# Kernel tuning notes

Hardware: AMD Instinct MI355X
Metric: run time of the kernel (lower is better)

Reference implementation:

```python
import jax, jax.numpy as jnp
import numpy as np

BATCH, S, N_DIM, B_SIZE = 512, 66, 304, 128

def setup_inputs() -> dict:
    key = jax.random.key(0)
    kx, kw = jax.random.split(key)
    x = jax.random.normal(kx, (BATCH, S, N_DIM), dtype=jnp.float32)
    W = jax.random.normal(kw, (B_SIZE, N_DIM), dtype=jnp.float32) * (1.0 / np.sqrt(N_DIM))
    b = jnp.zeros((B_SIZE,), dtype=jnp.float32)
    return {"x": x, "W": W, "b": b}

def reference(x, W, b):
    # Linear projection into tree space: (batch, S, B_size)
    t = jnp.einsum('bsd,kd->bsk', x, W) + b
    # Pairwise squared distances over sentence positions, same math as
    # expand/transpose/subtract/pow(2)/sum in the torch module.
    diff = t[:, :, None, :] - t[:, None, :, :]        # (batch, S, S, B_size)
    return jnp.sum(diff * diff, axis=-1)               # (batch, S, S)
```

## Files before the change

### kernel.cpp

```cpp
#include <hip/hip_runtime.h>
#include <hip/hip_bf16.h>

#define NBATCH 512
#define NS 66
#define ND 304
#define NK 128

#define XROWS 80
#define XSTRIDE_B 640
#define XBYTES (XROWS * XSTRIDE_B)
#define TSTRIDE_B 256
#define TBYTES (XROWS * TSTRIDE_B)
#define GSTRIDE 84

#define NTHREADS 512

typedef __attribute__((ext_vector_type(8))) short bf16x8;
typedef __attribute__((ext_vector_type(4))) short s16x4;
typedef __attribute__((ext_vector_type(4))) float f32x4;

__device__ __forceinline__ short f2bf(float x) {
    return __builtin_bit_cast(short, __float2bfloat16(x));
}

__global__ __launch_bounds__(NTHREADS, 4) void treeprobe_mfma(
    const float* __restrict__ x,
    const float* __restrict__ W,
    float* __restrict__ out)
{
    __shared__ __align__(16) char lds[XBYTES + TBYTES];
    char* const t_lds = lds + XBYTES;
    float* const G = (float*)lds;

    const int tid   = threadIdx.x;
    const int batch = blockIdx.x;
    const int lane  = tid & 63;
    const int wv    = tid >> 6;
    const int lr    = lane & 15;
    const int lg    = lane >> 4;

    bf16x8 wfrag[10];
    {
        const int c = wv * 16 + lr;
        const float* __restrict__ wr = W + c * ND;
#pragma unroll
        for (int kk = 0; kk < 10; ++kk) {
            const int k0 = kk * 32 + lg * 8;
            bf16x8 f = {0, 0, 0, 0, 0, 0, 0, 0};
            if (k0 < ND) {
                const float4 p0 = *reinterpret_cast<const float4*>(wr + k0);
                const float4 p1 = *reinterpret_cast<const float4*>(wr + k0 + 4);
                f[0] = f2bf(p0.x); f[1] = f2bf(p0.y);
                f[2] = f2bf(p0.z); f[3] = f2bf(p0.w);
                f[4] = f2bf(p1.x); f[5] = f2bf(p1.y);
                f[6] = f2bf(p1.z); f[7] = f2bf(p1.w);
            }
            wfrag[kk] = f;
        }
    }

    for (int i = tid; i < XBYTES / 16; i += NTHREADS) {
        *reinterpret_cast<f32x4*>(lds + i * 16) = (f32x4){0.f, 0.f, 0.f, 0.f};
    }
    __syncthreads();

    const float* __restrict__ xb = x + (size_t)batch * NS * ND;
    for (int e = tid; e < NS * ND / 4; e += NTHREADS) {
        const int s  = e / 76;
        const int d4 = (e % 76) * 4;
        const float4 v = *reinterpret_cast<const float4*>(xb + e * 4);
        int byte = s * XSTRIDE_B + d4 * 2;
        byte ^= (s & 7) << 4;
        s16x4 sv;
        sv[0] = f2bf(v.x); sv[1] = f2bf(v.y);
        sv[2] = f2bf(v.z); sv[3] = f2bf(v.w);
        *reinterpret_cast<s16x4*>(lds + byte) = sv;
    }
    __syncthreads();

    f32x4 acc[5];
#pragma unroll
    for (int mt = 0; mt < 5; ++mt) acc[mt] = (f32x4){0.f, 0.f, 0.f, 0.f};

#pragma unroll
    for (int kk = 0; kk < 10; ++kk) {
        bf16x8 a[5];
#pragma unroll
        for (int mt = 0; mt < 5; ++mt) {
            const int row = mt * 16 + lr;
            int byte = row * XSTRIDE_B + kk * 64 + lg * 16;
            byte ^= (row & 7) << 4;
            a[mt] = *reinterpret_cast<const bf16x8*>(lds + byte);
        }
#pragma unroll
        for (int mt = 0; mt < 5; ++mt)
            acc[mt] = __builtin_amdgcn_mfma_f32_16x16x32_bf16(
                a[mt], wfrag[kk], acc[mt], 0, 0, 0);
    }

    {
        const int col = wv * 16 + lr;
#pragma unroll
        for (int mt = 0; mt < 5; ++mt) {
#pragma unroll
            for (int r = 0; r < 4; ++r) {
                const int row = mt * 16 + lg * 4 + r;
                int byte = row * TSTRIDE_B + col * 2;
                byte ^= (row & 7) << 4;
                *reinterpret_cast<short*>(t_lds + byte) = f2bf(acc[mt][r]);
            }
        }
    }
    __syncthreads();

    for (int tile = wv; tile < 25; tile += 8) {
        const int ti = tile / 5, tj = tile % 5;
        f32x4 g = (f32x4){0.f, 0.f, 0.f, 0.f};
#pragma unroll
        for (int kk = 0; kk < 4; ++kk) {
            const int ra = ti * 16 + lr;
            int ba = ra * TSTRIDE_B + kk * 64 + lg * 16;
            ba ^= (ra & 7) << 4;
            const int rb = tj * 16 + lr;
            int bb = rb * TSTRIDE_B + kk * 64 + lg * 16;
            bb ^= (rb & 7) << 4;
            const bf16x8 av = *reinterpret_cast<const bf16x8*>(t_lds + ba);
            const bf16x8 bv = *reinterpret_cast<const bf16x8*>(t_lds + bb);
            g = __builtin_amdgcn_mfma_f32_16x16x32_bf16(av, bv, g, 0, 0, 0);
        }
#pragma unroll
        for (int r = 0; r < 4; ++r) {
            const int row = ti * 16 + lg * 4 + r;
            const int col = tj * 16 + lr;
            G[row * GSTRIDE + col] = g[r];
        }
    }
    __syncthreads();

    float* __restrict__ ob = out + (size_t)batch * NS * NS;
    for (int e = tid; e < NS * NS / 2; e += NTHREADS) {
        const int i = e / 33;
        const int j = (e % 33) * 2;
        const float nii = G[i * GSTRIDE + i];
        float2 r;
        r.x = nii + G[j * GSTRIDE + j] - 2.f * G[i * GSTRIDE + j];
        r.y = nii + G[(j + 1) * GSTRIDE + (j + 1)] - 2.f * G[i * GSTRIDE + j + 1];
        *reinterpret_cast<float2*>(ob + i * NS + j) = r;
    }
}

extern "C" void kernel_launch(void* const* d_in, const int* in_sizes, int n_in,
                              void* d_out, int out_size, void* d_ws, size_t ws_size,
                              hipStream_t stream) {
    const float* x = (const float*)d_in[0];
    const float* W = (const float*)d_in[1];
    float* out = (float*)d_out;

    treeprobe_mfma<<<NBATCH, NTHREADS, 0, stream>>>(x, W, out);
}
```

Before: 21.26 us.

## Pipeline x/W loads over K-chunks and exploit Gram symmetry with register epilogue

The kernel now uses 256 threads and splits the projection into ten K-chunks of 32. Global loads for x and W are issued two chunks ahead into registers and staged through a double-buffered LDS slice, so memory traffic overlaps the MFMA work and the LDS footprint shrinks. The Gram stage computes only the 15 upper-triangular 16x16 tiles and records the diagonal norms in a small array. Output is written straight from registers, with mirrored stores for off-diagonal tiles, replacing the full G matrix in LDS. The cost is more complex control flow, uncoalesced transposed stores, and reloading W from global per chunk instead of keeping it in registers.

```diff
diff --git a/kernel.cpp b/kernel.cpp
--- a/kernel.cpp
+++ b/kernel.cpp
@@ -5,15 +5,14 @@
 #define NS 66
 #define ND 304
 #define NK 128
-
-#define XROWS 80
-#define XSTRIDE_B 640
-#define XBYTES (XROWS * XSTRIDE_B)
+#define NTHREADS 256
+#define NCHUNK 10
+
+#define CSTRIDE_B 64
+#define CBYTES (80 * CSTRIDE_B)
 #define TSTRIDE_B 256
-#define TBYTES (XROWS * TSTRIDE_B)
-#define GSTRIDE 84
-
-#define NTHREADS 512
+#define TBYTES (80 * TSTRIDE_B)
+#define NE 528
 
 typedef __attribute__((ext_vector_type(8))) short bf16x8;
 typedef __attribute__((ext_vector_type(4))) short s16x4;
@@ -23,14 +22,19 @@
     return __builtin_bit_cast(short, __float2bfloat16(x));
 }
 
-__global__ __launch_bounds__(NTHREADS, 4) void treeprobe_mfma(
+__device__ const int TI_LUT[15] = {0,1,2,3,4, 0,0,0,0,1,1,1,2,2,3};
+__device__ const int TJ_LUT[15] = {0,1,2,3,4, 1,2,3,4,2,3,4,3,4,4};
+
+#define LDS_BARRIER() asm volatile("s_waitcnt lgkmcnt(0)\n\ts_barrier" ::: "memory")
+
+__global__ __launch_bounds__(NTHREADS, 2) void treeprobe_mfma(
     const float* __restrict__ x,
     const float* __restrict__ W,
     float* __restrict__ out)
 {
-    __shared__ __align__(16) char lds[XBYTES + TBYTES];
-    char* const t_lds = lds + XBYTES;
-    float* const G = (float*)lds;
+    __shared__ __align__(16) char xlds[2 * CBYTES];
+    __shared__ __align__(16) char t_lds[TBYTES];
+    __shared__ float norms[80];
 
     const int tid   = threadIdx.x;
     const int batch = blockIdx.x;
@@ -39,114 +43,183 @@
     const int lr    = lane & 15;
     const int lg    = lane >> 4;
 
-    bf16x8 wfrag[10];
-    {
-        const int c = wv * 16 + lr;
-        const float* __restrict__ wr = W + c * ND;
-#pragma unroll
-        for (int kk = 0; kk < 10; ++kk) {
-            const int k0 = kk * 32 + lg * 8;
-            bf16x8 f = {0, 0, 0, 0, 0, 0, 0, 0};
-            if (k0 < ND) {
-                const float4 p0 = *reinterpret_cast<const float4*>(wr + k0);
-                const float4 p1 = *reinterpret_cast<const float4*>(wr + k0 + 4);
-                f[0] = f2bf(p0.x); f[1] = f2bf(p0.y);
-                f[2] = f2bf(p0.z); f[3] = f2bf(p0.w);
-                f[4] = f2bf(p1.x); f[5] = f2bf(p1.y);
-                f[6] = f2bf(p1.z); f[7] = f2bf(p1.w);
-            }
-            wfrag[kk] = f;
-        }
-    }
-
-    for (int i = tid; i < XBYTES / 16; i += NTHREADS) {
-        *reinterpret_cast<f32x4*>(lds + i * 16) = (f32x4){0.f, 0.f, 0.f, 0.f};
-    }
-    __syncthreads();
-
     const float* __restrict__ xb = x + (size_t)batch * NS * ND;
-    for (int e = tid; e < NS * ND / 4; e += NTHREADS) {
-        const int s  = e / 76;
-        const int d4 = (e % 76) * 4;
-        const float4 v = *reinterpret_cast<const float4*>(xb + e * 4);
-        int byte = s * XSTRIDE_B + d4 * 2;
-        byte ^= (s & 7) << 4;
-        s16x4 sv;
-        sv[0] = f2bf(v.x); sv[1] = f2bf(v.y);
-        sv[2] = f2bf(v.z); sv[3] = f2bf(v.w);
-        *reinterpret_cast<s16x4*>(lds + byte) = sv;
-    }
-    __syncthreads();
-
-    f32x4 acc[5];
-#pragma unroll
-    for (int mt = 0; mt < 5; ++mt) acc[mt] = (f32x4){0.f, 0.f, 0.f, 0.f};
-
-#pragma unroll
-    for (int kk = 0; kk < 10; ++kk) {
-        bf16x8 a[5];
-#pragma unroll
-        for (int mt = 0; mt < 5; ++mt) {
-            const int row = mt * 16 + lr;
-            int byte = row * XSTRIDE_B + kk * 64 + lg * 16;
-            byte ^= (row & 7) << 4;
-            a[mt] = *reinterpret_cast<const bf16x8*>(lds + byte);
-        }
-#pragma unroll
-        for (int mt = 0; mt < 5; ++mt)
-            acc[mt] = __builtin_amdgcn_mfma_f32_16x16x32_bf16(
-                a[mt], wfrag[kk], acc[mt], 0, 0, 0);
-    }
-
-    {
-        const int col = wv * 16 + lr;
-#pragma unroll
-        for (int mt = 0; mt < 5; ++mt) {
+
+#define ISSUE_X(xr, c)                                                        \
+    _Pragma("unroll")                                                         \
+    for (int i = 0; i < 3; ++i) {                                             \
+        const int e = tid + i * NTHREADS;                                     \
+        float4 v = make_float4(0.f, 0.f, 0.f, 0.f);                           \
+        if (e < NE) {                                                         \
+            const int kc = (c) * 32 + (e & 7) * 4;                            \
+            if (kc < ND)                                                      \
+                v = *reinterpret_cast<const float4*>(xb + (e >> 3) * ND + kc);\
+        }                                                                     \
+        xr[i] = v;                                                            \
+    }
+
+#define ISSUE_W(wr4, c)                                                       \
+    _Pragma("unroll")                                                         \
+    for (int nt = 0; nt < 2; ++nt) {                                          \
+        const int row = (wv * 2 + nt) * 16 + lr;                              \
+        const int k0 = (c) * 32 + lg * 8;                                     \
+        if (k0 < ND) {                                                        \
+            wr4[nt * 2]     = *reinterpret_cast<const float4*>(W + row * ND + k0);     \
+            wr4[nt * 2 + 1] = *reinterpret_cast<const float4*>(W + row * ND + k0 + 4); \
+        } else {                                                              \
+            wr4[nt * 2]     = make_float4(0.f, 0.f, 0.f, 0.f);                \
+            wr4[nt * 2 + 1] = make_float4(0.f, 0.f, 0.f, 0.f);                \
+        }                                                                     \
+    }
+
+#define WRITE_X(xr, buf)                                                      \
+    _Pragma("unroll")                                                         \
+    for (int i = 0; i < 3; ++i) {                                             \
+        const int e = tid + i * NTHREADS;                                     \
+        if (e < NE) {                                                         \
+            const int row = e >> 3;                                           \
+            const int byte = row * CSTRIDE_B                                  \
+                + (((((e & 7) >> 1) ^ (row & 3)) << 4) | ((e & 1) << 3));     \
+            s16x4 sv;                                                         \
+            sv[0] = f2bf(xr[i].x); sv[1] = f2bf(xr[i].y);                     \
+            sv[2] = f2bf(xr[i].z); sv[3] = f2bf(xr[i].w);                     \
+            *reinterpret_cast<s16x4*>(xlds + (buf) * CBYTES + byte) = sv;     \
+        }                                                                     \
+    }
+
+#define CVT_W(wfrag, wr4)                                                     \
+    _Pragma("unroll")                                                         \
+    for (int nt = 0; nt < 2; ++nt) {                                          \
+        bf16x8 f;                                                             \
+        f[0] = f2bf(wr4[nt * 2].x);     f[1] = f2bf(wr4[nt * 2].y);           \
+        f[2] = f2bf(wr4[nt * 2].z);     f[3] = f2bf(wr4[nt * 2].w);           \
+        f[4] = f2bf(wr4[nt * 2 + 1].x); f[5] = f2bf(wr4[nt * 2 + 1].y);       \
+        f[6] = f2bf(wr4[nt * 2 + 1].z); f[7] = f2bf(wr4[nt * 2 + 1].w);       \
+        wfrag[nt] = f;                                                        \
+    }
+
+    float4 xr0[3], xr1[3], wr0[4], wr1[4];
+    ISSUE_X(xr0, 0); ISSUE_W(wr0, 0);
+    ISSUE_X(xr1, 1); ISSUE_W(wr1, 1);
+
+    for (int i = tid; i < 112; i += NTHREADS) {
+        const int b = i / 56;
+        const int r = 66 + (i % 56) / 4;
+        *reinterpret_cast<f32x4*>(xlds + b * CBYTES + r * CSTRIDE_B + (i % 4) * 16) =
+            (f32x4){0.f, 0.f, 0.f, 0.f};
+    }
+
+    WRITE_X(xr0, 0);
+    LDS_BARRIER();
+
+    f32x4 acc[5][2];
+#pragma unroll
+    for (int st = 0; st < 5; ++st) {
+        acc[st][0] = (f32x4){0.f, 0.f, 0.f, 0.f};
+        acc[st][1] = (f32x4){0.f, 0.f, 0.f, 0.f};
+    }
+
+    bf16x8 wfrag[2];
+#pragma unroll
+    for (int c = 0; c < NCHUNK; ++c) {
+        if ((c & 1) == 0) { CVT_W(wfrag, wr0); } else { CVT_W(wfrag, wr1); }
+
+        if (c + 2 < NCHUNK) {
+            if ((c & 1) == 0) { ISSUE_X(xr0, c + 2); ISSUE_W(wr0, c + 2); }
+            else              { ISSUE_X(xr1, c + 2); ISSUE_W(wr1, c + 2); }
+        }
+
+        {
+            const int cb = (c & 1) * CBYTES;
+#pragma unroll
+            for (int st = 0; st < 5; ++st) {
+                const int row = st * 16 + lr;
+                const int byte = cb + row * CSTRIDE_B + ((lg ^ (row & 3)) << 4);
+                const bf16x8 a = *reinterpret_cast<const bf16x8*>(xlds + byte);
+                acc[st][0] = __builtin_amdgcn_mfma_f32_16x16x32_bf16(
+                    wfrag[0], a, acc[st][0], 0, 0, 0);
+                acc[st][1] = __builtin_amdgcn_mfma_f32_16x16x32_bf16(
+                    wfrag[1], a, acc[st][1], 0, 0, 0);
+            }
+        }
+
+        if (c + 1 < NCHUNK) {
+            if (((c + 1) & 1) == 0) { WRITE_X(xr0, 0); }
+            else                    { WRITE_X(xr1, 1); }
+            LDS_BARRIER();
+        }
+    }
+
+#pragma unroll
+    for (int st = 0; st < 5; ++st) {
+        const int s = st * 16 + lr;
+#pragma unroll
+        for (int nt = 0; nt < 2; ++nt) {
+            const int c0 = (wv * 2 + nt) * 16 + lg * 4;
+            const int byte = (s * TSTRIDE_B + c0 * 2) ^ ((s & 7) << 4);
+            s16x4 sv;
+            sv[0] = f2bf(acc[st][nt][0]); sv[1] = f2bf(acc[st][nt][1]);
+            sv[2] = f2bf(acc[st][nt][2]); sv[3] = f2bf(acc[st][nt][3]);
+            *reinterpret_cast<s16x4*>(t_lds + byte) = sv;
+        }
+    }
+    LDS_BARRIER();
+
+    f32x4 g[4];
+    int ti[4], tj[4];
+    bool valid[4], isdiag[4];
+#pragma unroll
+    for (int si = 0; si < 4; ++si) {
+        const int pos = wv + si * 4;
+        valid[si] = pos < 15;
+        g[si] = (f32x4){0.f, 0.f, 0.f, 0.f};
+        ti[si] = 0; tj[si] = 0; isdiag[si] = false;
+        if (valid[si]) {
+            ti[si] = TI_LUT[pos]; tj[si] = TJ_LUT[pos];
+            isdiag[si] = pos < 5;
+#pragma unroll
+            for (int kk = 0; kk < 4; ++kk) {
+                const int ra = ti[si] * 16 + lr;
+                const int ba = (ra * TSTRIDE_B + kk * 64 + lg * 16) ^ ((ra & 7) << 4);
+                const int rb = tj[si] * 16 + lr;
+                const int bb = (rb * TSTRIDE_B + kk * 64 + lg * 16) ^ ((rb & 7) << 4);
+                g[si] = __builtin_amdgcn_mfma_f32_16x16x32_bf16(
+                    *reinterpret_cast<const bf16x8*>(t_lds + ba),
+                    *reinterpret_cast<const bf16x8*>(t_lds + bb), g[si], 0, 0, 0);
+            }
+            if (isdiag[si]) {
+#pragma unroll
+                for (int r = 0; r < 4; ++r)
+                    if (lr == lg * 4 + r) norms[ti[si] * 16 + lr] = g[si][r];
+            }
+        }
+    }
+    LDS_BARRIER();
+
+    float* __restrict__ ob = out + (size_t)batch * NS * NS;
+#pragma unroll
+    for (int si = 0; si < 4; ++si) {
+        if (valid[si]) {
+            const int j = tj[si] * 16 + lr;
+            const float nj = norms[j];
+            float v[4];
 #pragma unroll
             for (int r = 0; r < 4; ++r) {
-                const int row = mt * 16 + lg * 4 + r;
-                int byte = row * TSTRIDE_B + col * 2;
-                byte ^= (row & 7) << 4;
-                *reinterpret_cast<short*>(t_lds + byte) = f2bf(acc[mt][r]);
-            }
-        }
-    }
-    __syncthreads();
-
-    for (int tile = wv; tile < 25; tile += 8) {
-        const int ti = tile / 5, tj = tile % 5;
-        f32x4 g = (f32x4){0.f, 0.f, 0.f, 0.f};
-#pragma unroll
-        for (int kk = 0; kk < 4; ++kk) {
-            const int ra = ti * 16 + lr;
-            int ba = ra * TSTRIDE_B + kk * 64 + lg * 16;
-            ba ^= (ra & 7) << 4;
-            const int rb = tj * 16 + lr;
-            int bb = rb * TSTRIDE_B + kk * 64 + lg * 16;
-            bb ^= (rb & 7) << 4;
-            const bf16x8 av = *reinterpret_cast<const bf16x8*>(t_lds + ba);
-            const bf16x8 bv = *reinterpret_cast<const bf16x8*>(t_lds + bb);
-            g = __builtin_amdgcn_mfma_f32_16x16x32_bf16(av, bv, g, 0, 0, 0);
-        }
-#pragma unroll
-        for (int r = 0; r < 4; ++r) {
-            const int row = ti * 16 + lg * 4 + r;
-            const int col = tj * 16 + lr;
-            G[row * GSTRIDE + col] = g[r];
-        }
-    }
-    __syncthreads();
-
-    float* __restrict__ ob = out + (size_t)batch * NS * NS;
-    for (int e = tid; e < NS * NS / 2; e += NTHREADS) {
-        const int i = e / 33;
-        const int j = (e % 33) * 2;
-        const float nii = G[i * GSTRIDE + i];
-        float2 r;
-        r.x = nii + G[j * GSTRIDE + j] - 2.f * G[i * GSTRIDE + j];
-        r.y = nii + G[(j + 1) * GSTRIDE + (j + 1)] - 2.f * G[i * GSTRIDE + j + 1];
-        *reinterpret_cast<float2*>(ob + i * NS + j) = r;
-    }
+                const int i_ = ti[si] * 16 + lg * 4 + r;
+                v[r] = norms[i_] + nj - 2.f * g[si][r];
+                if (i_ < NS && j < NS) ob[i_ * NS + j] = v[r];
+            }
+            if (!isdiag[si] && j < NS) {
+                const int i0 = ti[si] * 16 + lg * 4;
+                *reinterpret_cast<float2*>(ob + j * NS + i0)     = make_float2(v[0], v[1]);
+                *reinterpret_cast<float2*>(ob + j * NS + i0 + 2) = make_float2(v[2], v[3]);
+            }
+        }
+    }
+#undef ISSUE_X
+#undef ISSUE_W
+#undef WRITE_X
+#undef CVT_W
 }
 
 extern "C" void kernel_launch(void* const* d_in, const int* in_sizes, int n_in,
```

After: 24.38 us. 1.15x slower.
